# Optimization experiments

Measured on AMD Instinct MI355X. Metric: run time of the kernel, lower is better.

Reference implementation:

```python
import jax, jax.numpy as jnp
import numpy as np

NUM = 21  # num_blurred_version


def _make_kernel(kp, p):
    # symmetrize: kernel + flip(rot90(kernel, 1, dims=[2,3]), dims=[2])
    k = kp + jnp.flip(jnp.rot90(kp, 1, axes=(2, 3)), axis=2)
    # reflect-pad right/bottom by p: (3,1,p+1,p+1) -> (3,1,2p+1,2p+1)
    k = jnp.pad(k, ((0, 0), (0, 0), (0, p), (0, p)), mode='reflect')
    s = 2 * p + 1
    k = jax.nn.softmax(k.reshape(3, 1, s * s), axis=2).reshape(3, 1, s, s)
    return k


def _dw_conv(x, k, p):
    # reflect-pad input by p on each spatial side, then depthwise (groups=3) conv
    xp = jnp.pad(x, ((0, 0), (0, 0), (p, p), (p, p)), mode='reflect')
    return jax.lax.conv_general_dilated(
        xp, k, window_strides=(1, 1), padding='VALID',
        dimension_numbers=('NCHW', 'OIHW', 'NCHW'), feature_group_count=3)


def setup_inputs() -> dict:
    key = jax.random.key(0)
    keys = jax.random.split(key, NUM + 1)
    inp = {"x": jax.random.normal(keys[0], (4, 3, 512, 512), dtype=jnp.float32)}
    for i in range(NUM):
        q = i + 2  # (kernel_size+1)//2 for kernel_size = 3+2i
        inp[f"k{i}"] = jax.random.uniform(keys[i + 1], (3, 1, q, q), dtype=jnp.float32)
    return inp


def reference(x, k0, k1, k2, k3, k4, k5, k6, k7, k8, k9, k10,
              k11, k12, k13, k14, k15, k16, k17, k18, k19, k20):
    kernels = [k0, k1, k2, k3, k4, k5, k6, k7, k8, k9, k10,
               k11, k12, k13, k14, k15, k16, k17, k18, k19, k20]
    res = [x]
    for i, kp in enumerate(kernels):
        p = i + 1  # kernel_padding
        k = _make_kernel(kp, p)
        res.append(_dw_conv(x, k, p))
    return jnp.concatenate(res, axis=1)  # (B, 3*(NUM+1), H, W)
```

## Files before the change

kernel.cpp:

```cpp
#include <hip/hip_runtime.h>
#include <cmath>

#define NUMB 21
#define HW (512*512)
#define OUTC 66

using short8 = __attribute__((ext_vector_type(8))) short;
using f32x4  = __attribute__((ext_vector_type(4))) float;

#define WSB4 12288u
#define PIMG_U4 211200u
#define WS_MID 3379200u
#define WS_NEEDED 10905600u

struct KPtrs { const float* k[NUMB]; };

__device__ __forceinline__ unsigned short f2bf(float f) {
  unsigned u = __builtin_bit_cast(unsigned, f);
  unsigned r = (u + 0x7fffu + ((u >> 16) & 1u)) >> 16;
  return (unsigned short)r;
}

__device__ __forceinline__ void nt_store4(const f32x4 v, float* p) {
  __builtin_nontemporal_store(v, (f32x4*)p);
}

__global__ __launch_bounds__(256) void weights_kernel(KPtrs kp, float* __restrict__ w) {
  const int bid = blockIdx.x;
  const int i = bid / 3, c = bid - 3 * (bid / 3);
  const int p = i + 1, s = 2 * p + 1, q = p + 1;
  int off = 0;
  for (int j = 0; j < i; ++j) { const int sj = 3 + 2 * j; off += 3 * sj * sj; }
  float* __restrict__ wd = w + off + c * s * s;
  const float* __restrict__ kc = kp.k[i] + c * q * q;
  const int n = s * s;
  const int tid = threadIdx.x;
  __shared__ float red[256];

  float m = -1e30f;
  for (int idx = tid; idx < n; idx += 256) {
    const int my = idx / s, nx = idx - my * s;
    const int a = min(my, 2 * p - my), bq = min(nx, 2 * p - nx);
    m = fmaxf(m, kc[a * q + bq] + kc[bq * q + a]);
  }
  red[tid] = m; __syncthreads();
  for (int st = 128; st > 0; st >>= 1) {
    if (tid < st) red[tid] = fmaxf(red[tid], red[tid + st]);
    __syncthreads();
  }
  const float vmax = red[0];
  __syncthreads();

  float sum = 0.f;
  for (int idx = tid; idx < n; idx += 256) {
    const int my = idx / s, nx = idx - my * s;
    const int a = min(my, 2 * p - my), bq = min(nx, 2 * p - nx);
    sum += expf(kc[a * q + bq] + kc[bq * q + a] - vmax);
  }
  red[tid] = sum; __syncthreads();
  for (int st = 128; st > 0; st >>= 1) {
    if (tid < st) red[tid] += red[tid + st];
    __syncthreads();
  }
  const float inv = 1.f / red[0];

  for (int idx = tid; idx < n; idx += 256) {
    const int my = idx / s, nx = idx - my * s;
    const int a = min(my, 2 * p - my), bq = min(nx, 2 * p - nx);
    wd[idx] = expf(kc[a * q + bq] + kc[bq * q + a] - vmax) * inv;
  }
}

__global__ __launch_bounds__(64) void pack_b2_kernel(const float* __restrict__ w,
                                                     uint4* __restrict__ ws) {
  const int gs = blockIdx.x;
  const int d  = blockIdx.y;
  const int c  = blockIdx.z;
  const int lane = threadIdx.x;
  int I0, CS, sb, ag;
  if (gs < 11)       { I0 = 1;  CS = 1; sb = 0;   ag = 3; }
  else if (gs < 49)  { I0 = 5;  CS = 2; sb = 11;  ag = 7; }
  else if (gs < 103) { I0 = 9;  CS = 2; sb = 49;  ag = 3; }
  else if (gs < 173) { I0 = 13; CS = 2; sb = 103; ag = 7; }
  else               { I0 = 17; CS = 2; sb = 173; ag = 3; }
  const int T = 2 * I0 + 9, PM = I0 + 4, STEPS = T * CS;
  const int ORI = PM + ag;
  const int q = gs - sb;
  const int t  = (CS == 2) ? (q >> 1) : q;
  const int cs = (CS == 2) ? (q & 1) : 0;
  const int n = lane & 15, g4 = lane >> 4;
  const int j = n >> 2, h = n & 3;
  const int i = I0 + j;
  const int p = i + 1, s = 2 * i + 3;
  int off = 0;
  for (int jj2 = 0; jj2 < i; ++jj2) { const int sj = 3 + 2 * jj2; off += 3 * sj * sj; }
  const float* __restrict__ wk = w + off + c * s * s;
  const int ky = t - PM + p;
  unsigned short hs[8];
#pragma unroll
  for (int jj = 0; jj < 8; ++jj) {
    const int k = 32 * cs + 8 * g4 + jj;
    const int kx = k - ORI - 4 * h - d + p;
    float v = 0.f;
    if (ky >= 0 && ky < s && kx >= 0 && kx < s) v = wk[ky * s + kx];
    hs[jj] = f2bf(v);
  }
  uint4 o;
  o.x = (unsigned)hs[0] | ((unsigned)hs[1] << 16);
  o.y = (unsigned)hs[2] | ((unsigned)hs[3] << 16);
  o.z = (unsigned)hs[4] | ((unsigned)hs[5] << 16);
  o.w = (unsigned)hs[6] | ((unsigned)hs[7] << 16);
  ws[(size_t)WSB4 + 768u * (unsigned)sb + (size_t)(((c * 4 + d) * STEPS + q) * 64 + lane)] = o;
}

__global__ __launch_bounds__(256) void pad_kernel(const float* __restrict__ x,
                                                  uint4* __restrict__ ws) {
  const int ch = blockIdx.y;
  const int chunk = blockIdx.x * 256 + threadIdx.x;
  if (chunk >= 39200) return;
  const int pr = chunk / 70, pc8 = (chunk - pr * 70) * 8;
  int gy = pr - 24; gy = gy < 0 ? -gy : gy; gy = gy > 511 ? 1022 - gy : gy;
  const float* __restrict__ row = x + (size_t)ch * HW + (size_t)gy * 512;
  unsigned short hs[8];
  if (pc8 >= 24 && pc8 <= 528) {
    const float4 v0 = *(const float4*)(row + pc8 - 24);
    const float4 v1 = *(const float4*)(row + pc8 - 20);
    hs[0] = f2bf(v0.x); hs[1] = f2bf(v0.y); hs[2] = f2bf(v0.z); hs[3] = f2bf(v0.w);
    hs[4] = f2bf(v1.x); hs[5] = f2bf(v1.y); hs[6] = f2bf(v1.z); hs[7] = f2bf(v1.w);
  } else {
#pragma unroll
    for (int j = 0; j < 8; ++j) {
      int gx = pc8 + j - 24; gx = gx < 0 ? -gx : gx; gx = gx > 511 ? 1022 - gx : gx;
      hs[j] = f2bf(row[gx]);
    }
  }
  uint4 o;
  o.x = (unsigned)hs[0] | ((unsigned)hs[1] << 16);
  o.y = (unsigned)hs[2] | ((unsigned)hs[3] << 16);
  o.z = (unsigned)hs[4] | ((unsigned)hs[5] << 16);
  o.w = (unsigned)hs[6] | ((unsigned)hs[7] << 16);
  ws[(size_t)PIMG_U4 + (size_t)ch * 39200 + chunk] = o;
}

__global__ __launch_bounds__(256) void copy_x_kernel(const f32x4* __restrict__ x,
                                                     f32x4* __restrict__ out) {
  const int idx = blockIdx.x * 256 + threadIdx.x;
  const int per_b = 3 * HW / 4;
  const int b = idx / per_b, r = idx - b * per_b;
  __builtin_nontemporal_store(x[idx], &out[(size_t)b * (OUTC * HW / 4) + r]);
}

template<int I0, int SB>
__device__ __forceinline__ void convg_compute_store(const int tid, const int b_, const int c,
    const int X0, const int Y0, const unsigned short* __restrict__ tile, float* __restrict__ ot,
    const uint4* __restrict__ wsb, float* __restrict__ out) {
  constexpr int T  = 2 * I0 + 9;
  constexpr int CS = (I0 == 1) ? 1 : 2;
  constexpr int C  = (CS == 1) ? 272 : 304;
  constexpr int CH0 = 3 + 3 * I0;
  constexpr int STEPS = T * CS;

  const int lane = tid & 63, d = tid >> 6;
  const int m = lane & 15, g4 = lane >> 4;
  const int abase = 16 * m + 8 * g4;
  const uint4* __restrict__ bl = wsb + (size_t)WSB4 + 768u * (unsigned)SB
                               + (size_t)((c * 4 + d) * STEPS) * 64 + lane;

  f32x4 acc[8];
#pragma unroll
  for (int yy = 0; yy < 8; ++yy) acc[yy] = (f32x4){0.f, 0.f, 0.f, 0.f};

  short8 awin[8][CS];
#pragma unroll
  for (int r = 0; r < 7; ++r)
#pragma unroll
    for (int cs2 = 0; cs2 < CS; ++cs2)
      awin[r][cs2] = *(const short8*)(tile + r * C + abase + 32 * cs2);

  short8 Bf[8][CS];
#pragma unroll
  for (int tt = 0; tt < 7; ++tt)
#pragma unroll
    for (int cs2 = 0; cs2 < CS; ++cs2)
      Bf[tt][cs2] = __builtin_bit_cast(short8, bl[(tt * CS + cs2) * 64]);

#pragma unroll
  for (int t = 0; t < T; ++t) {
#pragma unroll
    for (int cs2 = 0; cs2 < CS; ++cs2)
      awin[(t + 7) & 7][cs2] = *(const short8*)(tile + (t + 7) * C + abase + 32 * cs2);
    if (t + 7 < T) {
#pragma unroll
      for (int cs2 = 0; cs2 < CS; ++cs2)
        Bf[(t + 7) & 7][cs2] = __builtin_bit_cast(short8, bl[((t + 7) * CS + cs2) * 64]);
    }
#pragma unroll
    for (int yy = 0; yy < 8; ++yy)
#pragma unroll
      for (int cs2 = 0; cs2 < CS; ++cs2)
        acc[yy] = __builtin_amdgcn_mfma_f32_16x16x32_bf16(awin[(t + yy) & 7][cs2],
                                                          Bf[t & 7][cs2], acc[yy], 0, 0, 0);
  }

  __syncthreads();
  {
    const int n = lane & 15;
    const int j = n >> 2, h = n & 3;
#pragma unroll
    for (int yy = 0; yy < 8; ++yy) {
      float* orow = ot + (yy * 4 + j) * 260 + 64 * g4 + 4 * h + d;
#pragma unroll
      for (int r = 0; r < 4; ++r) orow[16 * r] = acc[yy][r];
    }
  }
  __syncthreads();
  {
    const int jw = tid >> 6;
    const int yy2 = (tid >> 3) & 7, xq = tid & 7;
    float* __restrict__ obase = out + ((size_t)(b_ * OUTC + CH0 + 3 * jw + c)) * HW
                              + (size_t)(Y0 + yy2) * 512 + X0;
    const float* __restrict__ srow = ot + (yy2 * 4 + jw) * 260;
#pragma unroll
    for (int v = 0; v < 8; ++v) {
      const int xo = 32 * v + 4 * xq;
      nt_store4(*(const f32x4*)(srow + xo), obase + xo);
    }
  }
}

template<int I0, int SB>
__device__ __forceinline__ void convg_body(const int lbid,
    const unsigned short* __restrict__ pimg, const uint4* __restrict__ wsb,
    float* __restrict__ out, char* smem) {
  constexpr int T  = 2 * I0 + 9;
  constexpr int CS = (I0 == 1) ? 1 : 2;
  constexpr int PM = I0 + 4;
  constexpr int AG = (8 - (PM & 7)) & 7;
  constexpr int ORI = PM + AG;
  constexpr int RT = T + 7;
  constexpr int C  = (CS == 1) ? 272 : 304;
  constexpr int CW8 = C / 8;
  constexpr int NIDX = RT * CW8;

  unsigned short* tile = (unsigned short*)smem;
  float* ot = (float*)smem;
  const int tid = threadIdx.x;
  const int bx = lbid & 1, by = (lbid >> 1) & 63, bz = lbid >> 7;
  const int b_ = bz / 3, c = bz - b_ * 3;
  const int X0 = bx * 256, Y0 = by * 8;

  const unsigned short* __restrict__ pb = pimg + (size_t)(b_ * 3 + c) * 313600
        + (size_t)(Y0 - PM + 24) * 560 + (X0 - ORI + 24);
  {
    const int wid = tid >> 6, lane = tid & 63;
    for (int base = wid * 64; base < NIDX; base += 256) {
      const int idx = base + lane;
      const int r = idx / CW8, cc = idx - r * CW8;
      const unsigned short* src = pb + r * 560 + cc * 8;
      unsigned short* dst = tile + (size_t)base * 8;
      if (idx < NIDX)
        __builtin_amdgcn_global_load_lds(
            (const __attribute__((address_space(1))) void*)src,
            (__attribute__((address_space(3))) void*)dst, 16, 0, 0);
    }
  }
  __syncthreads();
  convg_compute_store<I0, SB>(tid, b_, c, X0, Y0, tile, ot, wsb, out);
}

__global__ __launch_bounds__(256, 3) void convg_all_kernel(
    const unsigned short* __restrict__ pimg, const uint4* __restrict__ wsb,
    float* __restrict__ out) {
  __shared__ __align__(16) char smem[33280];
  const int gi = blockIdx.x;
  const int grp = gi / 1536;
  const int lb = gi - grp * 1536;
  const int lbid = (lb & 7) * 192 + (lb >> 3);
  if (grp == 0)      convg_body<17, 173>(lbid, pimg, wsb, out, smem);
  else if (grp == 1) convg_body<13, 103>(lbid, pimg, wsb, out, smem);
  else if (grp == 2) convg_body<9,  49 >(lbid, pimg, wsb, out, smem);
  else if (grp == 3) convg_body<5,  11 >(lbid, pimg, wsb, out, smem);
  else               convg_body<1,  0  >(lbid, pimg, wsb, out, smem);
}

template<int I0, int SB>
__global__ __launch_bounds__(256, 3) void convg_kernel(const float* __restrict__ xall,
                                                       const uint4* __restrict__ wsb,
                                                       float* __restrict__ out) {
  constexpr int T  = 2 * I0 + 9;
  constexpr int CS = (I0 == 1) ? 1 : 2;
  constexpr int PM = I0 + 4;
  constexpr int AG = (8 - (PM & 7)) & 7;
  constexpr int ORI = PM + AG;
  constexpr int RT = T + 7;
  constexpr int C  = (CS == 1) ? 272 : 304;

  __shared__ __align__(16) char smem[33280];
  unsigned short* tile = (unsigned short*)smem;
  float* ot = (float*)smem;

  const int tid = threadIdx.x;
  const int b_ = blockIdx.z / 3, c = blockIdx.z - b_ * 3;
  const int X0 = blockIdx.x * 256, Y0 = blockIdx.y * 8;
  const float* __restrict__ xin = xall + (size_t)(b_ * 3 + c) * HW;

  for (int idx = tid; idx < RT * C; idx += 256) {
    const int r = idx / C, e = idx - r * C;
    int gy = Y0 - PM + r; gy = gy < 0 ? -gy : gy; gy = gy > 511 ? 1022 - gy : gy;
    int gx = X0 - ORI + e; gx = gx < 0 ? -gx : gx; gx = gx > 511 ? 1022 - gx : gx;
    tile[idx] = f2bf(xin[gy * 512 + gx]);
  }
  __syncthreads();
  convg_compute_store<I0, SB>(tid, b_, c, X0, Y0, tile, ot, wsb, out);
}

template<int S>
__global__ __launch_bounds__(256) void conv_kernel(const float* __restrict__ xin_all,
                                                   const float* __restrict__ wg,
                                                   float* __restrict__ out, int ch0) {
  constexpr int P = (S - 1) / 2;
  constexpr int WHALO = 128 + 2 * P;
  constexpr int STRIDE = (WHALO + 3) & ~3;
  constexpr int HHALO = 32 + 2 * P;
  constexpr int NSEG = (S + 6) / 4;
  extern __shared__ float lds[];

  const int tx = threadIdx.x, ty = threadIdx.y;
  const int bz = blockIdx.z;
  const int b = bz / 3, c = bz - 3 * (bz / 3);
  const int x0 = blockIdx.x * 128, y0 = blockIdx.y * 32;
  const float* __restrict__ xin = xin_all + ((size_t)(b * 3 + c)) * HW;
  const float* __restrict__ wb = wg + c * (S * S);

  for (int ly = ty; ly < HHALO; ly += 8) {
    int gy = y0 - P + ly;
    gy = gy < 0 ? -gy : gy;
    gy = gy > 511 ? 1022 - gy : gy;
    const float* __restrict__ row = xin + (size_t)gy * 512;
    for (int lx = tx; lx < WHALO; lx += 32) {
      int gx = x0 - P + lx;
      gx = gx < 0 ? -gx : gx;
      gx = gx > 511 ? 1022 - gx : gx;
      lds[ly * STRIDE + lx] = row[gx];
    }
  }
  __syncthreads();

  float acc[4][4] = {};
  const int basecol = tx * 4;
  const int lrow0 = ty * 4;

#pragma unroll 1
  for (int ri = 0; ri < S + 3; ++ri) {
    float seg[NSEG * 4];
    const float* lp = &lds[(lrow0 + ri) * STRIDE + basecol];
#pragma unroll
    for (int j2 = 0; j2 < NSEG; ++j2) {
      const float4 v = *(const float4*)(lp + 4 * j2);
      seg[4 * j2 + 0] = v.x; seg[4 * j2 + 1] = v.y;
      seg[4 * j2 + 2] = v.z; seg[4 * j2 + 3] = v.w;
    }
#pragma unroll
    for (int r = 0; r < 4; ++r) {
      const int dy = ri - r;
      if (dy >= 0 && dy < S) {
        const float* __restrict__ wrow = wb + dy * S;
#pragma unroll
        for (int dx = 0; dx < S; ++dx) {
          const float wv = wrow[dx];
#pragma unroll
          for (int cc = 0; cc < 4; ++cc)
            acc[r][cc] = fmaf(wv, seg[dx + cc], acc[r][cc]);
        }
      }
    }
  }

  float* __restrict__ o = out + ((size_t)b * OUTC + (ch0 + c)) * HW
                        + (size_t)(y0 + lrow0) * 512 + (x0 + basecol);
#pragma unroll
  for (int r = 0; r < 4; ++r) {
    f32x4 v = (f32x4){acc[r][0], acc[r][1], acc[r][2], acc[r][3]};
    nt_store4(v, o + (size_t)r * 512);
  }
}

extern "C" void kernel_launch(void* const* d_in, const int* in_sizes, int n_in,
                              void* d_out, int out_size, void* d_ws, size_t ws_size,
                              hipStream_t stream) {
  (void)in_sizes; (void)n_in; (void)out_size;
  const float* x = (const float*)d_in[0];
  float* out = (float*)d_out;
  float* w = (float*)d_ws;

  KPtrs kp;
  for (int i = 0; i < NUMB; ++i) kp.k[i] = (const float*)d_in[1 + i];

  weights_kernel<<<dim3(63), dim3(256), 0, stream>>>(kp, w);
  copy_x_kernel<<<dim3(3072), dim3(256), 0, stream>>>((const f32x4*)x, (f32x4*)out);

  int offs[NUMB];
  { int off = 0; for (int i = 0; i < NUMB; ++i) { offs[i] = off; const int s = 3 + 2 * i; off += 3 * s * s; } }

#define LAUNCH_CONV(I) do { \
    constexpr int S_ = 3 + 2 * (I); \
    constexpr int P_ = (I) + 1; \
    constexpr int STRIDE_ = ((128 + 2 * P_) + 3) & ~3; \
    constexpr int HHALO_ = 32 + 2 * P_; \
    conv_kernel<S_><<<dim3(4, 16, 12), dim3(32, 8), (size_t)STRIDE_ * HHALO_ * sizeof(float), stream>>>( \
        x, w + offs[I], out, 3 + 3 * (I)); \
  } while (0)

  LAUNCH_CONV(0);

  if (ws_size >= WS_NEEDED) {
    pack_b2_kernel<<<dim3(259, 4, 3), dim3(64), 0, stream>>>(w, (uint4*)d_ws);
    pad_kernel<<<dim3(154, 12), dim3(256), 0, stream>>>(x, (uint4*)d_ws);
    const unsigned short* pimg = (const unsigned short*)((const uint4*)d_ws + PIMG_U4);
    convg_all_kernel<<<dim3(7680), dim3(256), 0, stream>>>(pimg, (const uint4*)d_ws, out);
  } else if (ws_size >= WS_MID) {
    pack_b2_kernel<<<dim3(259, 4, 3), dim3(64), 0, stream>>>(w, (uint4*)d_ws);
    convg_kernel<17, 173><<<dim3(2, 64, 12), dim3(256), 0, stream>>>(x, (const uint4*)d_ws, out);
    convg_kernel<13, 103><<<dim3(2, 64, 12), dim3(256), 0, stream>>>(x, (const uint4*)d_ws, out);
    convg_kernel<9,  49 ><<<dim3(2, 64, 12), dim3(256), 0, stream>>>(x, (const uint4*)d_ws, out);
    convg_kernel<5,  11 ><<<dim3(2, 64, 12), dim3(256), 0, stream>>>(x, (const uint4*)d_ws, out);
    convg_kernel<1,  0  ><<<dim3(2, 64, 12), dim3(256), 0, stream>>>(x, (const uint4*)d_ws, out);
  } else {
    LAUNCH_CONV(1);  LAUNCH_CONV(2);  LAUNCH_CONV(3);  LAUNCH_CONV(4);
    LAUNCH_CONV(5);  LAUNCH_CONV(6);  LAUNCH_CONV(7);  LAUNCH_CONV(8);
    LAUNCH_CONV(9);  LAUNCH_CONV(10); LAUNCH_CONV(11); LAUNCH_CONV(12);
    LAUNCH_CONV(13); LAUNCH_CONV(14); LAUNCH_CONV(15); LAUNCH_CONV(16);
    LAUNCH_CONV(17); LAUNCH_CONV(18); LAUNCH_CONV(19); LAUNCH_CONV(20);
  }
#undef LAUNCH_CONV
}
```

Baseline: 181.9 us.

## Split LDS tile load into stages overlapped with MFMA compute; fuse x copy into pad

The grouped conv body now issues the global-to-LDS tile loads in two batches. It prefetches the first weight fragments between them and waits with explicit vmcnt counts, so the MFMA loop over the first rows starts before the whole tile has arrived. The second half runs after a second partial wait. Separately, the passthrough copy of x into the output is folded into the padding kernel, which removes one launch and one extra read of x. The hand-tuned vmcnt constants depend on instruction ordering and are fragile if the compiler reorders or adds memory operations.

Result: slower. 187.8 us (+3.3%).

```diff
diff --git a/kernel.cpp b/kernel.cpp
--- a/kernel.cpp
+++ b/kernel.cpp
@@ -23,6 +23,18 @@
 
 __device__ __forceinline__ void nt_store4(const f32x4 v, float* p) {
   __builtin_nontemporal_store(v, (f32x4*)p);
+}
+
+template<int N> __device__ __forceinline__ void wait_vmcnt() {
+  if constexpr      (N == 4)  asm volatile("s_waitcnt vmcnt(4)"  ::: "memory");
+  else if constexpr (N == 8)  asm volatile("s_waitcnt vmcnt(8)"  ::: "memory");
+  else if constexpr (N == 12) asm volatile("s_waitcnt vmcnt(12)" ::: "memory");
+  else if constexpr (N == 16) asm volatile("s_waitcnt vmcnt(16)" ::: "memory");
+  else if constexpr (N == 17) asm volatile("s_waitcnt vmcnt(17)" ::: "memory");
+  else if constexpr (N == 18) asm volatile("s_waitcnt vmcnt(18)" ::: "memory");
+  else if constexpr (N == 26) asm volatile("s_waitcnt vmcnt(26)" ::: "memory");
+  else if constexpr (N == 38) asm volatile("s_waitcnt vmcnt(38)" ::: "memory");
+  else static_assert(N == 4, "add vmcnt case");
 }
 
 __global__ __launch_bounds__(256) void weights_kernel(KPtrs kp, float* __restrict__ w) {
@@ -113,8 +125,9 @@
   ws[(size_t)WSB4 + 768u * (unsigned)sb + (size_t)(((c * 4 + d) * STEPS + q) * 64 + lane)] = o;
 }
 
-__global__ __launch_bounds__(256) void pad_kernel(const float* __restrict__ x,
-                                                  uint4* __restrict__ ws) {
+__global__ __launch_bounds__(256) void pad_copy_kernel(const float* __restrict__ x,
+                                                       uint4* __restrict__ ws,
+                                                       float* __restrict__ out) {
   const int ch = blockIdx.y;
   const int chunk = blockIdx.x * 256 + threadIdx.x;
   if (chunk >= 39200) return;
@@ -123,10 +136,15 @@
   const float* __restrict__ row = x + (size_t)ch * HW + (size_t)gy * 512;
   unsigned short hs[8];
   if (pc8 >= 24 && pc8 <= 528) {
-    const float4 v0 = *(const float4*)(row + pc8 - 24);
-    const float4 v1 = *(const float4*)(row + pc8 - 20);
+    const f32x4 v0 = *(const f32x4*)(row + pc8 - 24);
+    const f32x4 v1 = *(const f32x4*)(row + pc8 - 20);
     hs[0] = f2bf(v0.x); hs[1] = f2bf(v0.y); hs[2] = f2bf(v0.z); hs[3] = f2bf(v0.w);
     hs[4] = f2bf(v1.x); hs[5] = f2bf(v1.y); hs[6] = f2bf(v1.z); hs[7] = f2bf(v1.w);
+    if (pr >= 24 && pr < 536) {
+      const int b = ch / 3, c = ch - 3 * (ch / 3);
+      float* o = out + ((size_t)(b * OUTC + c)) * HW + (size_t)(pr - 24) * 512 + (pc8 - 24);
+      nt_store4(v0, o); nt_store4(v1, o + 4);
+    }
   } else {
 #pragma unroll
     for (int j = 0; j < 8; ++j) {
@@ -241,6 +259,17 @@
   constexpr int C  = (CS == 1) ? 272 : 304;
   constexpr int CW8 = C / 8;
   constexpr int NIDX = RT * CW8;
+  constexpr int NP   = (NIDX + 255) & ~255;
+  constexpr int IPW  = NP / 256;
+  constexpr int K1   = (IPW + 1) / 2;
+  constexpr int ROWS_A = (256 * K1) / CW8;
+  constexpr int T1   = (ROWS_A - 7 < T) ? (ROWS_A - 7) : T;
+  constexpr int LB1  = (T1 < T - 7) ? T1 : (T - 7);
+  constexpr int CNT1 = 7 * CS + (IPW - K1);
+  constexpr int CNT2 = LB1 * CS;
+  constexpr int CH0 = 3 + 3 * I0;
+  constexpr int STEPS = T * CS;
+  static_assert(NP * 16 <= 33280, "tile overflow");
 
   unsigned short* tile = (unsigned short*)smem;
   float* ot = (float*)smem;
@@ -249,23 +278,123 @@
   const int b_ = bz / 3, c = bz - b_ * 3;
   const int X0 = bx * 256, Y0 = by * 8;
 
+  const int lane = tid & 63, wid = tid >> 6;
   const unsigned short* __restrict__ pb = pimg + (size_t)(b_ * 3 + c) * 313600
         + (size_t)(Y0 - PM + 24) * 560 + (X0 - ORI + 24);
+
+#pragma unroll
+  for (int k = 0; k < K1; ++k) {
+    const int base = wid * 64 + 256 * k;
+    const int idx = base + lane;
+    const int r = idx / CW8, cc = idx - r * CW8;
+    const unsigned short* src = (idx < NIDX) ? (pb + r * 560 + cc * 8) : pb;
+    __builtin_amdgcn_global_load_lds(
+        (const __attribute__((address_space(1))) void*)src,
+        (__attribute__((address_space(3))) void*)(tile + (size_t)base * 8), 16, 0, 0);
+  }
+  asm volatile("" ::: "memory");
+
+  const int d = wid;
+  const int m = lane & 15, g4 = lane >> 4;
+  const int abase = 16 * m + 8 * g4;
+  const uint4* __restrict__ bl = wsb + (size_t)WSB4 + 768u * (unsigned)SB
+                               + (size_t)((c * 4 + d) * STEPS) * 64 + lane;
+  short8 Bf[8][CS];
+#pragma unroll
+  for (int tt = 0; tt < 7; ++tt)
+#pragma unroll
+    for (int cs2 = 0; cs2 < CS; ++cs2)
+      Bf[tt][cs2] = __builtin_bit_cast(short8, bl[(tt * CS + cs2) * 64]);
+  asm volatile("" ::: "memory");
+
+#pragma unroll
+  for (int k = K1; k < IPW; ++k) {
+    const int base = wid * 64 + 256 * k;
+    const int idx = base + lane;
+    const int r = idx / CW8, cc = idx - r * CW8;
+    const unsigned short* src = (idx < NIDX) ? (pb + r * 560 + cc * 8) : pb;
+    __builtin_amdgcn_global_load_lds(
+        (const __attribute__((address_space(1))) void*)src,
+        (__attribute__((address_space(3))) void*)(tile + (size_t)base * 8), 16, 0, 0);
+  }
+  wait_vmcnt<CNT1>();
+  __builtin_amdgcn_s_barrier();
+  asm volatile("" ::: "memory");
+
+  f32x4 acc[8];
+#pragma unroll
+  for (int yy = 0; yy < 8; ++yy) acc[yy] = (f32x4){0.f, 0.f, 0.f, 0.f};
+
+  short8 awin[8][CS];
+#pragma unroll
+  for (int r = 0; r < 7; ++r)
+#pragma unroll
+    for (int cs2 = 0; cs2 < CS; ++cs2)
+      awin[r][cs2] = *(const short8*)(tile + r * C + abase + 32 * cs2);
+
+#pragma unroll
+  for (int t = 0; t < T1; ++t) {
+#pragma unroll
+    for (int cs2 = 0; cs2 < CS; ++cs2)
+      awin[(t + 7) & 7][cs2] = *(const short8*)(tile + (t + 7) * C + abase + 32 * cs2);
+    if (t + 7 < T) {
+#pragma unroll
+      for (int cs2 = 0; cs2 < CS; ++cs2)
+        Bf[(t + 7) & 7][cs2] = __builtin_bit_cast(short8, bl[((t + 7) * CS + cs2) * 64]);
+    }
+#pragma unroll
+    for (int yy = 0; yy < 8; ++yy)
+#pragma unroll
+      for (int cs2 = 0; cs2 < CS; ++cs2)
+        acc[yy] = __builtin_amdgcn_mfma_f32_16x16x32_bf16(awin[(t + yy) & 7][cs2],
+                                                          Bf[t & 7][cs2], acc[yy], 0, 0, 0);
+  }
+  wait_vmcnt<CNT2>();
+  __builtin_amdgcn_s_barrier();
+  asm volatile("" ::: "memory");
+
+#pragma unroll
+  for (int t = T1; t < T; ++t) {
+#pragma unroll
+    for (int cs2 = 0; cs2 < CS; ++cs2)
+      awin[(t + 7) & 7][cs2] = *(const short8*)(tile + (t + 7) * C + abase + 32 * cs2);
+    if (t + 7 < T) {
+#pragma unroll
+      for (int cs2 = 0; cs2 < CS; ++cs2)
+        Bf[(t + 7) & 7][cs2] = __builtin_bit_cast(short8, bl[((t + 7) * CS + cs2) * 64]);
+    }
+#pragma unroll
+    for (int yy = 0; yy < 8; ++yy)
+#pragma unroll
+      for (int cs2 = 0; cs2 < CS; ++cs2)
+        acc[yy] = __builtin_amdgcn_mfma_f32_16x16x32_bf16(awin[(t + yy) & 7][cs2],
+                                                          Bf[t & 7][cs2], acc[yy], 0, 0, 0);
+  }
+
+  __syncthreads();
   {
-    const int wid = tid >> 6, lane = tid & 63;
-    for (int base = wid * 64; base < NIDX; base += 256) {
-      const int idx = base + lane;
-      const int r = idx / CW8, cc = idx - r * CW8;
-      const unsigned short* src = pb + r * 560 + cc * 8;
-      unsigned short* dst = tile + (size_t)base * 8;
-      if (idx < NIDX)
-        __builtin_amdgcn_global_load_lds(
-            (const __attribute__((address_space(1))) void*)src,
-            (__attribute__((address_space(3))) void*)dst, 16, 0, 0);
-    }
-  }
-  __syncthreads();
-  convg_compute_store<I0, SB>(tid, b_, c, X0, Y0, tile, ot, wsb, out);
+    const int n = lane & 15;
+    const int j = n >> 2, h = n & 3;
+#pragma unroll
+    for (int yy = 0; yy < 8; ++yy) {
+      float* orow = ot + (yy * 4 + j) * 260 + 64 * g4 + 4 * h + d;
+#pragma unroll
+      for (int r = 0; r < 4; ++r) orow[16 * r] = acc[yy][r];
+    }
+  }
+  __syncthreads();
+  {
+    const int jw = tid >> 6;
+    const int yy2 = (tid >> 3) & 7, xq = tid & 7;
+    float* __restrict__ obase = out + ((size_t)(b_ * OUTC + CH0 + 3 * jw + c)) * HW
+                              + (size_t)(Y0 + yy2) * 512 + X0;
+    const float* __restrict__ srow = ot + (yy2 * 4 + jw) * 260;
+#pragma unroll
+    for (int v = 0; v < 8; ++v) {
+      const int xo = 32 * v + 4 * xq;
+      nt_store4(*(const f32x4*)(srow + xo), obase + xo);
+    }
+  }
 }
 
 __global__ __launch_bounds__(256, 3) void convg_all_kernel(
@@ -397,7 +526,6 @@
   for (int i = 0; i < NUMB; ++i) kp.k[i] = (const float*)d_in[1 + i];
 
   weights_kernel<<<dim3(63), dim3(256), 0, stream>>>(kp, w);
-  copy_x_kernel<<<dim3(3072), dim3(256), 0, stream>>>((const f32x4*)x, (f32x4*)out);
 
   int offs[NUMB];
   { int off = 0; for (int i = 0; i < NUMB; ++i) { offs[i] = off; const int s = 3 + 2 * i; off += 3 * s * s; } }
@@ -414,11 +542,12 @@
   LAUNCH_CONV(0);
 
   if (ws_size >= WS_NEEDED) {
+    pad_copy_kernel<<<dim3(154, 12), dim3(256), 0, stream>>>(x, (uint4*)d_ws, out);
     pack_b2_kernel<<<dim3(259, 4, 3), dim3(64), 0, stream>>>(w, (uint4*)d_ws);
-    pad_kernel<<<dim3(154, 12), dim3(256), 0, stream>>>(x, (uint4*)d_ws);
     const unsigned short* pimg = (const unsigned short*)((const uint4*)d_ws + PIMG_U4);
     convg_all_kernel<<<dim3(7680), dim3(256), 0, stream>>>(pimg, (const uint4*)d_ws, out);
   } else if (ws_size >= WS_MID) {
+    copy_x_kernel<<<dim3(3072), dim3(256), 0, stream>>>((const f32x4*)x, (f32x4*)out);
     pack_b2_kernel<<<dim3(259, 4, 3), dim3(64), 0, stream>>>(w, (uint4*)d_ws);
     convg_kernel<17, 173><<<dim3(2, 64, 12), dim3(256), 0, stream>>>(x, (const uint4*)d_ws, out);
     convg_kernel<13, 103><<<dim3(2, 64, 12), dim3(256), 0, stream>>>(x, (const uint4*)d_ws, out);
@@ -426,6 +555,7 @@
     convg_kernel<5,  11 ><<<dim3(2, 64, 12), dim3(256), 0, stream>>>(x, (const uint4*)d_ws, out);
     convg_kernel<1,  0  ><<<dim3(2, 64, 12), dim3(256), 0, stream>>>(x, (const uint4*)d_ws, out);
   } else {
+    copy_x_kernel<<<dim3(3072), dim3(256), 0, stream>>>((const f32x4*)x, (f32x4*)out);
     LAUNCH_CONV(1);  LAUNCH_CONV(2);  LAUNCH_CONV(3);  LAUNCH_CONV(4);
     LAUNCH_CONV(5);  LAUNCH_CONV(6);  LAUNCH_CONV(7);  LAUNCH_CONV(8);
     LAUNCH_CONV(9);  LAUNCH_CONV(10); LAUNCH_CONV(11); LAUNCH_CONV(12);
```

## Fuse x copy into pad kernel and trim B prefetch and LDS for occupancy

Applied to the files above, without the earlier changes.

Folds the identity copy of x into the output into the bf16 padding kernel, so the interior float4 loads are reused and one full pass over x is dropped. In the MFMA conv, the B-fragment prefetch ring shrinks from 8 to 4 stages and the output staging is split into two halves, which lets LDS shrink to 32 KiB. Launch bounds are raised from 3 to 5 blocks per SM for the main conv. These changes aim to raise occupancy and cut register and LDS pressure, at the cost of shallower weight prefetch and one extra barrier pair.

New measurement: 654.5 us. 260% more time.

```diff
diff --git a/kernel.cpp b/kernel.cpp
--- a/kernel.cpp
+++ b/kernel.cpp
@@ -113,8 +113,9 @@
   ws[(size_t)WSB4 + 768u * (unsigned)sb + (size_t)(((c * 4 + d) * STEPS + q) * 64 + lane)] = o;
 }
 
-__global__ __launch_bounds__(256) void pad_kernel(const float* __restrict__ x,
-                                                  uint4* __restrict__ ws) {
+__global__ __launch_bounds__(256) void pad_copy_kernel(const float* __restrict__ x,
+                                                       uint4* __restrict__ ws,
+                                                       float* __restrict__ out) {
   const int ch = blockIdx.y;
   const int chunk = blockIdx.x * 256 + threadIdx.x;
   if (chunk >= 39200) return;
@@ -123,10 +124,15 @@
   const float* __restrict__ row = x + (size_t)ch * HW + (size_t)gy * 512;
   unsigned short hs[8];
   if (pc8 >= 24 && pc8 <= 528) {
-    const float4 v0 = *(const float4*)(row + pc8 - 24);
-    const float4 v1 = *(const float4*)(row + pc8 - 20);
+    const f32x4 v0 = *(const f32x4*)(row + pc8 - 24);
+    const f32x4 v1 = *(const f32x4*)(row + pc8 - 20);
     hs[0] = f2bf(v0.x); hs[1] = f2bf(v0.y); hs[2] = f2bf(v0.z); hs[3] = f2bf(v0.w);
     hs[4] = f2bf(v1.x); hs[5] = f2bf(v1.y); hs[6] = f2bf(v1.z); hs[7] = f2bf(v1.w);
+    if (pr >= 24 && pr < 536) {
+      const int b = ch / 3, c = ch - 3 * (ch / 3);
+      float* o = out + ((size_t)(b * OUTC + c)) * HW + (size_t)(pr - 24) * 512 + (pc8 - 24);
+      nt_store4(v0, o); nt_store4(v1, o + 4);
+    }
   } else {
 #pragma unroll
     for (int j = 0; j < 8; ++j) {
@@ -177,9 +183,9 @@
     for (int cs2 = 0; cs2 < CS; ++cs2)
       awin[r][cs2] = *(const short8*)(tile + r * C + abase + 32 * cs2);
 
-  short8 Bf[8][CS];
-#pragma unroll
-  for (int tt = 0; tt < 7; ++tt)
+  short8 Bf[4][CS];
+#pragma unroll
+  for (int tt = 0; tt < 3; ++tt)
 #pragma unroll
     for (int cs2 = 0; cs2 < CS; ++cs2)
       Bf[tt][cs2] = __builtin_bit_cast(short8, bl[(tt * CS + cs2) * 64]);
@@ -189,41 +195,45 @@
 #pragma unroll
     for (int cs2 = 0; cs2 < CS; ++cs2)
       awin[(t + 7) & 7][cs2] = *(const short8*)(tile + (t + 7) * C + abase + 32 * cs2);
-    if (t + 7 < T) {
+    if (t + 3 < T) {
 #pragma unroll
       for (int cs2 = 0; cs2 < CS; ++cs2)
-        Bf[(t + 7) & 7][cs2] = __builtin_bit_cast(short8, bl[((t + 7) * CS + cs2) * 64]);
+        Bf[(t + 3) & 3][cs2] = __builtin_bit_cast(short8, bl[((t + 3) * CS + cs2) * 64]);
     }
 #pragma unroll
     for (int yy = 0; yy < 8; ++yy)
 #pragma unroll
       for (int cs2 = 0; cs2 < CS; ++cs2)
         acc[yy] = __builtin_amdgcn_mfma_f32_16x16x32_bf16(awin[(t + yy) & 7][cs2],
-                                                          Bf[t & 7][cs2], acc[yy], 0, 0, 0);
-  }
-
-  __syncthreads();
-  {
-    const int n = lane & 15;
-    const int j = n >> 2, h = n & 3;
-#pragma unroll
-    for (int yy = 0; yy < 8; ++yy) {
-      float* orow = ot + (yy * 4 + j) * 260 + 64 * g4 + 4 * h + d;
-#pragma unroll
-      for (int r = 0; r < 4; ++r) orow[16 * r] = acc[yy][r];
-    }
-  }
-  __syncthreads();
-  {
-    const int jw = tid >> 6;
-    const int yy2 = (tid >> 3) & 7, xq = tid & 7;
-    float* __restrict__ obase = out + ((size_t)(b_ * OUTC + CH0 + 3 * jw + c)) * HW
-                              + (size_t)(Y0 + yy2) * 512 + X0;
-    const float* __restrict__ srow = ot + (yy2 * 4 + jw) * 260;
-#pragma unroll
-    for (int v = 0; v < 8; ++v) {
-      const int xo = 32 * v + 4 * xq;
-      nt_store4(*(const f32x4*)(srow + xo), obase + xo);
+                                                          Bf[t & 3][cs2], acc[yy], 0, 0, 0);
+  }
+
+#pragma unroll
+  for (int H = 0; H < 2; ++H) {
+    __syncthreads();
+    {
+      const int n = lane & 15;
+      const int j = n >> 2, h = n & 3;
+#pragma unroll
+      for (int q = 0; q < 4; ++q) {
+        float* orow = ot + (q * 4 + j) * 260 + 64 * g4 + 4 * h + d;
+        const int yy = H * 4 + q;
+#pragma unroll
+        for (int r = 0; r < 4; ++r) orow[16 * r] = acc[yy][r];
+      }
+    }
+    __syncthreads();
+    {
+      const int jw = tid >> 6, rem = tid & 63;
+      const int yy2l = rem >> 4, xq2 = rem & 15;
+      float* __restrict__ obase = out + ((size_t)(b_ * OUTC + CH0 + 3 * jw + c)) * HW
+                                + (size_t)(Y0 + H * 4 + yy2l) * 512 + X0;
+      const float* __restrict__ srow = ot + (yy2l * 4 + jw) * 260;
+#pragma unroll
+      for (int v = 0; v < 4; ++v) {
+        const int xo = v * 64 + 4 * xq2;
+        nt_store4(*(const f32x4*)(srow + xo), obase + xo);
+      }
     }
   }
 }
@@ -241,6 +251,7 @@
   constexpr int C  = (CS == 1) ? 272 : 304;
   constexpr int CW8 = C / 8;
   constexpr int NIDX = RT * CW8;
+  static_assert(NIDX * 16 <= 32768, "tile overflow");
 
   unsigned short* tile = (unsigned short*)smem;
   float* ot = (float*)smem;
@@ -268,10 +279,10 @@
   convg_compute_store<I0, SB>(tid, b_, c, X0, Y0, tile, ot, wsb, out);
 }
 
-__global__ __launch_bounds__(256, 3) void convg_all_kernel(
+__global__ __launch_bounds__(256, 5) void convg_all_kernel(
     const unsigned short* __restrict__ pimg, const uint4* __restrict__ wsb,
     float* __restrict__ out) {
-  __shared__ __align__(16) char smem[33280];
+  __shared__ __align__(16) char smem[32768];
   const int gi = blockIdx.x;
   const int grp = gi / 1536;
   const int lb = gi - grp * 1536;
@@ -295,7 +306,7 @@
   constexpr int RT = T + 7;
   constexpr int C  = (CS == 1) ? 272 : 304;
 
-  __shared__ __align__(16) char smem[33280];
+  __shared__ __align__(16) char smem[32768];
   unsigned short* tile = (unsigned short*)smem;
   float* ot = (float*)smem;
 
@@ -397,7 +408,6 @@
   for (int i = 0; i < NUMB; ++i) kp.k[i] = (const float*)d_in[1 + i];
 
   weights_kernel<<<dim3(63), dim3(256), 0, stream>>>(kp, w);
-  copy_x_kernel<<<dim3(3072), dim3(256), 0, stream>>>((const f32x4*)x, (f32x4*)out);
 
   int offs[NUMB];
   { int off = 0; for (int i = 0; i < NUMB; ++i) { offs[i] = off; const int s = 3 + 2 * i; off += 3 * s * s; } }
@@ -414,11 +424,12 @@
   LAUNCH_CONV(0);
 
   if (ws_size >= WS_NEEDED) {
+    pad_copy_kernel<<<dim3(154, 12), dim3(256), 0, stream>>>(x, (uint4*)d_ws, out);
     pack_b2_kernel<<<dim3(259, 4, 3), dim3(64), 0, stream>>>(w, (uint4*)d_ws);
-    pad_kernel<<<dim3(154, 12), dim3(256), 0, stream>>>(x, (uint4*)d_ws);
     const unsigned short* pimg = (const unsigned short*)((const uint4*)d_ws + PIMG_U4);
     convg_all_kernel<<<dim3(7680), dim3(256), 0, stream>>>(pimg, (const uint4*)d_ws, out);
   } else if (ws_size >= WS_MID) {
+    copy_x_kernel<<<dim3(3072), dim3(256), 0, stream>>>((const f32x4*)x, (f32x4*)out);
     pack_b2_kernel<<<dim3(259, 4, 3), dim3(64), 0, stream>>>(w, (uint4*)d_ws);
     convg_kernel<17, 173><<<dim3(2, 64, 12), dim3(256), 0, stream>>>(x, (const uint4*)d_ws, out);
     convg_kernel<13, 103><<<dim3(2, 64, 12), dim3(256), 0, stream>>>(x, (const uint4*)d_ws, out);
@@ -426,6 +437,7 @@
     convg_kernel<5,  11 ><<<dim3(2, 64, 12), dim3(256), 0, stream>>>(x, (const uint4*)d_ws, out);
     convg_kernel<1,  0  ><<<dim3(2, 64, 12), dim3(256), 0, stream>>>(x, (const uint4*)d_ws, out);
   } else {
+    copy_x_kernel<<<dim3(3072), dim3(256), 0, stream>>>((const f32x4*)x, (f32x4*)out);
     LAUNCH_CONV(1);  LAUNCH_CONV(2);  LAUNCH_CONV(3);  LAUNCH_CONV(4);
     LAUNCH_CONV(5);  LAUNCH_CONV(6);  LAUNCH_CONV(7);  LAUNCH_CONV(8);
     LAUNCH_CONV(9);  LAUNCH_CONV(10); LAUNCH_CONV(11); LAUNCH_CONV(12);
```
